# Performance work log

Measured on AMD Instinct MI355X. Metric: run time of the kernel, lower is better.

The kernel has to match this reference:

```python
import jax, jax.numpy as jnp
import numpy as np

B, SEQ, EMB, LAT = 8192, 1024, 768, 256
TAXA = ['phylum', 'order', 'family', 'genus', 'species']
NC = {'phylum': 40, 'order': 200, 'family': 800, 'genus': 3000, 'species': 12000}


def _table(P, C):
    # parent->child validity: child c belongs to parent (c % P); every parent non-empty
    return (jnp.arange(C)[None, :] % P) == jnp.arange(P)[:, None]


def setup_inputs() -> dict:
    key = jax.random.key(0)
    ks = jax.random.split(key, 16)
    d = {}
    d['sequences'] = jax.random.normal(ks[0], (B, SEQ), jnp.float32)
    d['W_dnabert'] = jax.random.normal(ks[1], (SEQ, EMB), jnp.float32) * 0.02
    d['W_enc'] = jax.random.normal(ks[2], (EMB, LAT), jnp.float32) * 0.02
    for i, t in enumerate(TAXA):
        d[f'W_cls_{t}'] = jax.random.normal(ks[3 + i], (LAT, NC[t]), jnp.float32) * 0.02
        d[f'W_dec_{t}'] = jax.random.normal(ks[8 + i], (LAT, EMB), jnp.float32) * 0.02
    d['W_global'] = jax.random.normal(ks[13], (LAT, EMB), jnp.float32) * 0.02
    d['T_order'] = _table(NC['phylum'], NC['order'])
    d['T_family'] = _table(NC['order'], NC['family'])
    d['T_genus'] = _table(NC['family'], NC['genus'])
    d['T_species'] = _table(NC['genus'], NC['species'])
    return d


def reference(sequences, W_dnabert, W_enc,
              W_cls_phylum, W_cls_order, W_cls_family, W_cls_genus, W_cls_species,
              W_dec_phylum, W_dec_order, W_dec_family, W_dec_genus, W_dec_species,
              W_global, T_order, T_family, T_genus, T_species):
    # frozen dnabert (torch.no_grad)
    emb = jax.lax.stop_gradient(sequences @ W_dnabert)          # [B, EMB]
    z = emb @ W_enc                                             # [B, LAT]

    Wc = {'phylum': W_cls_phylum, 'order': W_cls_order, 'family': W_cls_family,
          'genus': W_cls_genus, 'species': W_cls_species}
    Wd = {'phylum': W_dec_phylum, 'order': W_dec_order, 'family': W_dec_family,
          'genus': W_dec_genus, 'species': W_dec_species}
    Tt = {'order': T_order, 'family': T_family, 'genus': T_genus, 'species': T_species}

    logits_out, recon_out = {}, {}
    parent_preds = None
    for taxon in TAXA:
        logits = z @ Wc[taxon]                                  # [B, C_taxon]
        if parent_preds is not None and taxon in Tt:
            # vectorized hierarchical mask: gather valid-class row per sample
            mask = Tt[taxon][parent_preds]                      # [B, C_taxon] bool
            logits = jnp.where(mask, logits, -jnp.inf)
        logits_out[taxon] = logits
        recon_out[taxon] = z @ Wd[taxon]                        # [B, EMB]
        parent_preds = jnp.argmax(logits, axis=1)               # [B] int

    global_rec = z @ W_global                                   # [B, EMB]
    return (z,
            logits_out['phylum'], logits_out['order'], logits_out['family'],
            logits_out['genus'], logits_out['species'],
            recon_out['phylum'], recon_out['order'], recon_out['family'],
            recon_out['genus'], recon_out['species'],
            global_rec, emb)
```

## Files before the change

kernel.cpp:

```cpp
#include <hip/hip_runtime.h>
#include <hip/hip_bf16.h>

typedef __attribute__((ext_vector_type(8))) short short8;
typedef __attribute__((ext_vector_type(4))) float f32x4;
typedef unsigned short ushort_t;
typedef unsigned int u32;

static constexpr int Bn  = 8192;
static constexpr int SEQ = 1024;
static constexpr int EMB = 768;
static constexpr int LAT = 256;

static constexpr size_t OFF_Z   = 0;
static constexpr size_t OFF_LP  = 2097152;
static constexpr size_t OFF_LO  = 2424832;
static constexpr size_t OFF_LF  = 4063232;
static constexpr size_t OFF_LG  = 10616832;
static constexpr size_t OFF_LS  = 35192832;
static constexpr size_t OFF_RP  = 133496832;
static constexpr size_t OFF_EMB = 171245568;

static constexpr size_t SCR      = OFF_LO;
static constexpr size_t S_SEQ_H  = SCR + 0;
static constexpr size_t S_SEQ_L  = SCR + 4194304;
static constexpr size_t S_EMB_H  = SCR + 8388608;
static constexpr size_t S_EMB_L  = SCR + 11534336;
static constexpr size_t S_Z_H    = SCR + 14680064;
static constexpr size_t S_Z_L    = SCR + 15728640;
static constexpr size_t S_REC_H  = SCR + 16777216;
static constexpr size_t S_REC_L  = SCR + 17367040;
static constexpr size_t S_CLS_T  = SCR + 17956864;
static constexpr size_t S_T_O    = S_CLS_T + 0;
static constexpr size_t S_T_F    = S_CLS_T + 51200;
static constexpr size_t S_T_G    = S_CLS_T + 256000;
static constexpr size_t S_T_S    = S_CLS_T + 1024000;

static constexpr size_t SCR_END  = SCR + 22052864;
static constexpr size_t TE0 = 0,        TE1 = 9418752;
static constexpr size_t TZ0 = 9418752,  TZ1 = 18837504;
static constexpr size_t TR0 = 18837504, TR1 = 27254784;
static constexpr size_t FILLZ_N4 = 8388608 / 4;
static constexpr size_t FILLR_N4 = (14680064 - 8388608) / 4;
static constexpr size_t ZREC_N4  = (17956864 - 14680064) / 4;
static constexpr size_t CLST_N4  = (22052864 - 17956864) / 4;

static constexpr size_t WS_DNA_H = 0;
static constexpr size_t WS_DNA_L = 786432;
static constexpr size_t WS_ENC_H = 1572864;
static constexpr size_t WS_ENC_L = 1769472;
static constexpr size_t WS_COMPACT_FL = 983040;

#define MASKED_VAL (-1.0e30f)

__device__ __forceinline__ ushort_t bfbits(float f) {
    return __builtin_bit_cast(ushort_t, __float2bfloat16(f));
}
__device__ __forceinline__ float bf2f(ushort_t h) {
    return __builtin_bit_cast(float, ((unsigned)h) << 16);
}
__device__ __forceinline__ void split2(float f, ushort_t& h, ushort_t& l) {
    h = bfbits(f);
    l = bfbits(f - bf2f(h));
}

__device__ __forceinline__ size_t tile_pos(int rt, int nKT, int kt, int r, int g) {
    return ((size_t)rt * nKT + kt) * 8192 + (size_t)r * 64 + ((g ^ (r & 7)) << 3);
}

__device__ __forceinline__ void fill_span(f32x4* __restrict__ dst, size_t n4,
                                          int fb, int nFB)
{
    const f32x4 v = {MASKED_VAL, MASKED_VAL, MASKED_VAL, MASKED_VAL};
    for (size_t i = (size_t)fb * 256 + threadIdx.x; i < n4; i += (size_t)nFB * 256)
        __builtin_nontemporal_store(v, dst + i);
}

__global__ __launch_bounds__(256)
void fill_kernel(f32x4* __restrict__ dst, size_t n4)
{
    fill_span(dst, n4, blockIdx.x, gridDim.x);
}

__device__ __forceinline__ void prep_wtT_body(const float* __restrict__ src,
                                              ushort_t* __restrict__ dh,
                                              ushort_t* __restrict__ dl,
                                              int K, int N, int bx, int nb)
{
    const int gpr = K >> 3, nKT = K >> 6;
    const int nG = N * gpr;
    for (int gi = bx * 256 + threadIdx.x; gi < nG; gi += nb * 256) {
        const int n = gi / gpr, gk = gi - n * gpr;
        short8 hh, ll;
        #pragma unroll
        for (int j = 0; j < 8; ++j) {
            ushort_t hv, lv;
            split2(src[(size_t)(gk * 8 + j) * N + n], hv, lv);
            hh[j] = (short)hv; ll[j] = (short)lv;
        }
        const size_t base = tile_pos(n >> 7, nKT, gk >> 3, n & 127, gk & 7);
        *(short8*)(dh + base) = hh;
        *(short8*)(dl + base) = ll;
    }
}

struct Ptr6 { const float* p[6]; };

__device__ __forceinline__ void prep_rec_body(Ptr6 s, ushort_t* __restrict__ dh,
                                              ushort_t* __restrict__ dl, int bx, int nb)
{
    constexpr int gpr = 32, nKT = 4;
    const int nG = 4608 * gpr;
    for (int gi = bx * 256 + threadIdx.x; gi < nG; gi += nb * 256) {
        const int np = gi / gpr, gk = gi - np * gpr;
        const int m = np / 768, nn = np - m * 768;
        const float* sm = s.p[m];
        short8 hh, ll;
        #pragma unroll
        for (int j = 0; j < 8; ++j) {
            ushort_t hv, lv;
            split2(sm[(size_t)(gk * 8 + j) * 768 + nn], hv, lv);
            hh[j] = (short)hv; ll[j] = (short)lv;
        }
        const size_t base = tile_pos(np >> 7, nKT, gk >> 3, np & 127, gk & 7);
        *(short8*)(dh + base) = hh;
        *(short8*)(dl + base) = ll;
    }
}

__device__ __forceinline__ void transpose_body(float t[64][65], int bx,
    const float* __restrict__ Wo, const float* __restrict__ Wf,
    const float* __restrict__ Wg, const float* __restrict__ Ws,
    float* To, float* Tf, float* Tg, float* Ts)
{
    const float* src; float* dst; int C; int cb;
    if (bx < 16)       { src = Wo; dst = To; C = 200;   cb = bx; }
    else if (bx < 68)  { src = Wf; dst = Tf; C = 800;   cb = bx - 16; }
    else if (bx < 256) { src = Wg; dst = Tg; C = 3000;  cb = bx - 68; }
    else               { src = Ws; dst = Ts; C = 12000; cb = bx - 256; }
    const int ct = cb >> 2, kt = cb & 3;
    const int c0 = ct * 64;
    const int tid = threadIdx.x;
    const int cl = tid & 63, kr = tid >> 6;
    #pragma unroll
    for (int i = 0; i < 16; ++i) {
        const int k = i * 4 + kr;
        const int c = c0 + cl;
        t[k][cl] = (c < C) ? src[(size_t)(kt * 64 + k) * C + c] : 0.f;
    }
    __syncthreads();
    #pragma unroll
    for (int i = 0; i < 16; ++i) {
        const int cc = i * 4 + kr;
        const int c = c0 + cc;
        if (c < C) dst[(size_t)c * 256 + kt * 64 + cl] = t[cl][cc];
    }
}

__device__ __forceinline__ void split_body(const float* __restrict__ src,
                                           ushort_t* __restrict__ dh,
                                           ushort_t* __restrict__ dl,
                                           int M, int K, int bx, int nb)
{
    const int gpr = K >> 3, nKT = K >> 6;
    const int nG = M * gpr;
    for (int gi = bx * 256 + threadIdx.x; gi < nG; gi += nb * 256) {
        const int row = gi / gpr, gk = gi - row * gpr;
        const float* s = src + (size_t)row * K + gk * 8;
        const float4 a = *(const float4*)s;
        const float4 b = *(const float4*)(s + 4);
        const float f[8] = {a.x, a.y, a.z, a.w, b.x, b.y, b.z, b.w};
        short8 hh, ll;
        #pragma unroll
        for (int j = 0; j < 8; ++j) {
            ushort_t hv, lv;
            split2(f[j], hv, lv);
            hh[j] = (short)hv; ll[j] = (short)lv;
        }
        const size_t base = tile_pos(row >> 7, nKT, gk >> 3, row & 127, gk & 7);
        *(short8*)(dh + base) = hh;
        *(short8*)(dl + base) = ll;
    }
}

__global__ __launch_bounds__(256)
void prep_everything(const float* Wdna, ushort_t* dnaH, ushort_t* dnaL,
                     const float* Wenc, ushort_t* encH, ushort_t* encL,
                     Ptr6 s6, ushort_t* recH, ushort_t* recL,
                     const float* Wo, const float* Wf, const float* Wg, const float* Ws,
                     float* To, float* Tf, float* Tg, float* Ts,
                     const float* seq, ushort_t* seqH, ushort_t* seqL)
{
    __shared__ float t[64][65];
    const int bx = blockIdx.x;
    if (bx < 1056) {
        if (bx < 384)       prep_wtT_body(Wdna, dnaH, dnaL, 1024, 768, bx, 384);
        else if (bx < 480)  prep_wtT_body(Wenc, encH, encL, 768, 256, bx - 384, 96);
        else                prep_rec_body(s6, recH, recL, bx - 480, 576);
    } else if (bx < 2064) {
        transpose_body(t, bx - 1056, Wo, Wf, Wg, Ws, To, Tf, Tg, Ts);
    } else {
        split_body(seq, seqH, seqL, Bn, SEQ, bx - 2064, 4096);
    }
}

__device__ __forceinline__ void gload16(const ushort_t* g, ushort_t* l) {
    __builtin_amdgcn_global_load_lds(
        (const __attribute__((address_space(1))) u32*)g,
        (__attribute__((address_space(3))) u32*)l, 16, 0, 0);
}

__global__ __launch_bounds__(256)
void gemm_ts_fill(const ushort_t* __restrict__ Ahg, const ushort_t* __restrict__ Alg,
                  const ushort_t* __restrict__ Bhg, const ushort_t* __restrict__ Blg,
                  int K, float* __restrict__ Cbase, int chunkW, size_t chunkStride,
                  int nCT, int nGB,
                  f32x4* __restrict__ f1, size_t n1,
                  f32x4* __restrict__ f2, size_t n2)
{
    __shared__ ushort_t sAh[8192], sAl[8192], sBh[8192], sBl[8192];

    if ((int)blockIdx.x >= nGB) {
        const int fb = blockIdx.x - nGB, nFB = gridDim.x - nGB;
        fill_span(f1, n1, fb, nFB);
        if (n2) fill_span(f2, n2, fb, nFB);
        return;
    }

    const int tid = threadIdx.x, w = tid >> 6, lane = tid & 63;
    const int wm = w >> 1, wn = w & 1;
    const int fr = lane & 15, kg = lane >> 4;
    const int nKT = K >> 6;
    const int rt = blockIdx.x / nCT, ct = blockIdx.x % nCT;
    const int col0 = ct * 128;
    const int chunk = col0 / chunkW;
    const int lc0 = col0 - chunk * chunkW;
    float* __restrict__ C = Cbase + (size_t)chunk * chunkStride;

    const int sbase = w * 2048;
    const int lgo = lane * 8;

    f32x4 acc[4][4] = {};

    for (int kt = 0; kt < nKT; ++kt) {
        const size_t at = ((size_t)rt * nKT + kt) * 8192;
        const size_t bt = ((size_t)ct * nKT + kt) * 8192;
        #pragma unroll
        for (int i = 0; i < 4; ++i) {
            const int co = sbase + i * 512;
            gload16(Ahg + at + co + lgo, &sAh[co]);
            gload16(Alg + at + co + lgo, &sAl[co]);
            gload16(Bhg + bt + co + lgo, &sBh[co]);
            gload16(Blg + bt + co + lgo, &sBl[co]);
        }
        __syncthreads();

        #pragma unroll
        for (int ks = 0; ks < 2; ++ks) {
            const int g = ks * 4 + kg;
            short8 a_h[4], a_l[4], b_h[4], b_l[4];
            #pragma unroll
            for (int i = 0; i < 4; ++i) {
                const int ra = wm * 64 + i * 16 + fr;
                const int pa = ra * 64 + ((g ^ (ra & 7)) << 3);
                a_h[i] = *(const short8*)&sAh[pa];
                a_l[i] = *(const short8*)&sAl[pa];
                const int rb = wn * 64 + i * 16 + fr;
                const int pb = rb * 64 + ((g ^ (rb & 7)) << 3);
                b_h[i] = *(const short8*)&sBh[pb];
                b_l[i] = *(const short8*)&sBl[pb];
            }
            #pragma unroll
            for (int mi = 0; mi < 4; ++mi) {
                #pragma unroll
                for (int ni = 0; ni < 4; ++ni) {
                    acc[mi][ni] = __builtin_amdgcn_mfma_f32_16x16x32_bf16(a_h[mi], b_h[ni], acc[mi][ni], 0, 0, 0);
                    acc[mi][ni] = __builtin_amdgcn_mfma_f32_16x16x32_bf16(a_h[mi], b_l[ni], acc[mi][ni], 0, 0, 0);
                    acc[mi][ni] = __builtin_amdgcn_mfma_f32_16x16x32_bf16(a_l[mi], b_h[ni], acc[mi][ni], 0, 0, 0);
                }
            }
        }
        __syncthreads();
    }

    const int crow = kg * 4;
    #pragma unroll
    for (int mi = 0; mi < 4; ++mi) {
        const int gr = rt * 128 + wm * 64 + mi * 16 + crow;
        #pragma unroll
        for (int ni = 0; ni < 4; ++ni) {
            const int gc = lc0 + wn * 64 + ni * 16 + fr;
            #pragma unroll
            for (int j = 0; j < 4; ++j)
                C[(size_t)(gr + j) * chunkW + gc] = acc[mi][ni][j];
        }
    }
}

__global__ __launch_bounds__(256)
void split_tiled(const float* __restrict__ src, ushort_t* __restrict__ dh,
                 ushort_t* __restrict__ dl, int M, int K)
{
    split_body(src, dh, dl, M, K, blockIdx.x, gridDim.x);
}

template <int C, int P>
__device__ __forceinline__ int level_w(const float* __restrict__ WT,
                                       float4 zr, int p, int lane,
                                       float* __restrict__ rec )
{
    const int cnt = (C - p + P - 1) / P;
    float sv[5];
    #pragma unroll
    for (int j = 0; j < 5; ++j) {
        float s = 0.f;
        if (j < cnt) {
            const float4 wv = *(const float4*)(WT + (size_t)(p + j * P) * 256 + lane * 4);
            s = fmaf(wv.x, zr.x, fmaf(wv.y, zr.y, fmaf(wv.z, zr.z, wv.w * zr.w)));
        }
        sv[j] = s;
    }
    #pragma unroll
    for (int j = 0; j < 5; ++j) {
        if (j < cnt) {
            #pragma unroll
            for (int off = 32; off; off >>= 1) sv[j] += __shfl_xor(sv[j], off);
        }
    }
    float best = sv[0];
    int bj = 0;
    #pragma unroll
    for (int j = 1; j < 5; ++j)
        if (j < cnt && sv[j] > best) { best = sv[j]; bj = j; }

    if (lane == 0) {
        rec[0] = __int_as_float(p);
        rec[1] = sv[0];
        rec[2] = (1 < cnt) ? sv[1] : 0.f;
        rec[3] = (2 < cnt) ? sv[2] : 0.f;
        rec[4] = (3 < cnt) ? sv[3] : 0.f;
        rec[5] = (4 < cnt) ? sv[4] : 0.f;
    }
    return p + bj * P;
}

__device__ __forceinline__ void chain_body(float* zsh, int bid,
    const float* __restrict__ z, const float* __restrict__ Wp,
    const float* __restrict__ ToT, const float* __restrict__ TfT,
    const float* __restrict__ TgT, const float* __restrict__ TsT,
    float* __restrict__ out, float* __restrict__ compact)
{
    const int w    = threadIdx.x >> 6;
    const int lane = threadIdx.x & 63;
    const size_t b = (size_t)bid * 4 + w;

    const float4 zr4 = *(const float4*)(z + b * 256 + lane * 4);
    *(float4*)&zsh[w * 256 + lane * 4] = zr4;
    asm volatile("s_waitcnt lgkmcnt(0)" ::: "memory");
    const float* zrow = zsh + w * 256;

    float pv = MASKED_VAL;
    if (lane < 40) {
        float s0 = 0.f, s1 = 0.f, s2 = 0.f, s3 = 0.f;
        #pragma unroll 4
        for (int k = 0; k < 256; k += 4) {
            s0 = fmaf(zrow[k + 0], Wp[(k + 0) * 40 + lane], s0);
            s1 = fmaf(zrow[k + 1], Wp[(k + 1) * 40 + lane], s1);
            s2 = fmaf(zrow[k + 2], Wp[(k + 2) * 40 + lane], s2);
            s3 = fmaf(zrow[k + 3], Wp[(k + 3) * 40 + lane], s3);
        }
        pv = (s0 + s1) + (s2 + s3);
        out[OFF_LP + b * 40 + lane] = pv;
    }
    float v = pv;
    int idx = lane;
    #pragma unroll
    for (int off = 32; off; off >>= 1) {
        float ov = __shfl_xor(v, off);
        int   oi = __shfl_xor(idx, off);
        if (ov > v || (ov == v && oi < idx)) { v = ov; idx = oi; }
    }
    int p = idx;

    p = level_w<200, 40>    (ToT, zr4, p, lane, compact + (0 * Bn + b) * 6);
    p = level_w<800, 200>   (TfT, zr4, p, lane, compact + (1 * Bn + b) * 6);
    p = level_w<3000, 800>  (TgT, zr4, p, lane, compact + (2 * Bn + b) * 6);
    (void)level_w<12000, 3000>(TsT, zr4, p, lane, compact + (3 * Bn + b) * 6);
}

__global__ __launch_bounds__(256)
void chain_fill(const float* __restrict__ z, const float* __restrict__ Wp,
                const float* __restrict__ ToT, const float* __restrict__ TfT,
                const float* __restrict__ TgT, const float* __restrict__ TsT,
                float* __restrict__ out, float* __restrict__ compact,
                f32x4* __restrict__ f1, size_t n1)
{
    __shared__ float zsh[4 * 256];
    const int bx = blockIdx.x;
    if (bx >= Bn / 4) {
        fill_span(f1, n1, bx - Bn / 4, gridDim.x - Bn / 4);
        return;
    }
    chain_body(zsh, bx, z, Wp, ToT, TfT, TgT, TsT, out, compact);
}

__global__ __launch_bounds__(256)
void scatter_kernel(const float* __restrict__ compact, float* __restrict__ out)
{
    const int t = blockIdx.x * 256 + threadIdx.x;
    if (t >= 4 * Bn) return;
    const int lvl = t >> 13, b = t & (Bn - 1);
    const int Cs[4] = {200, 800, 3000, 12000};
    const int Ps[4] = {40, 200, 800, 3000};
    const size_t OFFL[4] = {OFF_LO, OFF_LF, OFF_LG, OFF_LS};
    const float* rec = compact + ((size_t)lvl * Bn + b) * 6;
    const int p = __float_as_int(rec[0]);
    const int C = Cs[lvl], P = Ps[lvl];
    const int cnt = (C - p + P - 1) / P;
    float* dst = out + OFFL[lvl] + (size_t)b * C;
    for (int j = 0; j < cnt; ++j)
        dst[p + j * P] = rec[1 + j];
}

extern "C" void kernel_launch(void* const* d_in, const int* in_sizes, int n_in,
                              void* d_out, int out_size, void* d_ws, size_t ws_size,
                              hipStream_t stream)
{
    const float* seq    = (const float*)d_in[0];
    const float* Wdna   = (const float*)d_in[1];
    const float* Wenc   = (const float*)d_in[2];
    const float* Wcls_p = (const float*)d_in[3];
    const float* Wdec_p = (const float*)d_in[4];
    const float* Wcls_o = (const float*)d_in[5];
    const float* Wdec_o = (const float*)d_in[6];
    const float* Wcls_f = (const float*)d_in[7];
    const float* Wdec_f = (const float*)d_in[8];
    const float* Wcls_g = (const float*)d_in[9];
    const float* Wdec_g = (const float*)d_in[10];
    const float* Wcls_s = (const float*)d_in[11];
    const float* Wdec_s = (const float*)d_in[12];
    const float* Wglob  = (const float*)d_in[13];
    (void)in_sizes; (void)n_in; (void)out_size; (void)ws_size;

    float* out = (float*)d_out;
    ushort_t* ws = (ushort_t*)d_ws;

    ushort_t* seqH = (ushort_t*)(out + S_SEQ_H);
    ushort_t* seqL = (ushort_t*)(out + S_SEQ_L);
    ushort_t* embH = (ushort_t*)(out + S_EMB_H);
    ushort_t* embL = (ushort_t*)(out + S_EMB_L);
    ushort_t* zH   = (ushort_t*)(out + S_Z_H);
    ushort_t* zL   = (ushort_t*)(out + S_Z_L);
    ushort_t* recH = (ushort_t*)(out + S_REC_H);
    ushort_t* recL = (ushort_t*)(out + S_REC_L);
    float* ToT = out + S_T_O;
    float* TfT = out + S_T_F;
    float* TgT = out + S_T_G;
    float* TsT = out + S_T_S;
    ushort_t* dnaH = ws + WS_DNA_H;
    ushort_t* dnaL = ws + WS_DNA_L;
    ushort_t* encH = ws + WS_ENC_H;
    ushort_t* encL = ws + WS_ENC_L;
    float* compact = (float*)ws + WS_COMPACT_FL;
    f32x4* tail = (f32x4*)(out + SCR_END);

    Ptr6 s6{{Wdec_p, Wdec_o, Wdec_f, Wdec_g, Wdec_s, Wglob}};
    prep_everything<<<6160, 256, 0, stream>>>(
        Wdna, dnaH, dnaL, Wenc, encH, encL, s6, recH, recL,
        Wcls_o, Wcls_f, Wcls_g, Wcls_s, ToT, TfT, TgT, TsT,
        seq, seqH, seqL);

    gemm_ts_fill<<<384 + 1664, 256, 0, stream>>>(
        seqH, seqL, dnaH, dnaL, SEQ, out + OFF_EMB, EMB, 0, 6, 384,
        tail + TE0, TE1 - TE0, nullptr, 0);
    split_tiled<<<3072, 256, 0, stream>>>(out + OFF_EMB, embH, embL, Bn, EMB);

    gemm_ts_fill<<<128 + 896, 256, 0, stream>>>(
        embH, embL, encH, encL, EMB, out + OFF_Z, LAT, 0, 2, 128,
        (f32x4*)(out + SCR), FILLZ_N4, tail + TZ0, TZ1 - TZ0);
    split_tiled<<<1024, 256, 0, stream>>>(out + OFF_Z, zH, zL, Bn, LAT);

    gemm_ts_fill<<<2304 + 768, 256, 0, stream>>>(
        zH, zL, recH, recL, LAT, out + OFF_RP, EMB, (size_t)Bn * EMB, 36, 2304,
        (f32x4*)(out + S_EMB_H), FILLR_N4, tail + TR0, TR1 - TR0);

    chain_fill<<<2048 + 512, 256, 0, stream>>>(out + OFF_Z, Wcls_p, ToT, TfT,
                                               TgT, TsT, out, compact,
                                               (f32x4*)(out + S_Z_H), ZREC_N4);

    fill_kernel<<<512, 256, 0, stream>>>((f32x4*)(out + S_CLS_T), CLST_N4);
    scatter_kernel<<<128, 256, 0, stream>>>(compact, out);
}
```

Baseline: 304.8 us.

## Swizzle GEMM block order, nontemporal recon stores, merge fill into scatter

```diff
diff --git a/kernel.cpp b/kernel.cpp
--- a/kernel.cpp
+++ b/kernel.cpp
@@ -213,7 +213,7 @@
 void gemm_ts_fill(const ushort_t* __restrict__ Ahg, const ushort_t* __restrict__ Alg,
                   const ushort_t* __restrict__ Bhg, const ushort_t* __restrict__ Blg,
                   int K, float* __restrict__ Cbase, int chunkW, size_t chunkStride,
-                  int nCT, int nGB,
+                  int nCT, int nGB, int ntC,
                   f32x4* __restrict__ f1, size_t n1,
                   f32x4* __restrict__ f2, size_t n2)
 {
@@ -226,11 +226,13 @@
         return;
     }
 
+    const int bx = (blockIdx.x & 7) * (nGB >> 3) + (blockIdx.x >> 3);
+
     const int tid = threadIdx.x, w = tid >> 6, lane = tid & 63;
     const int wm = w >> 1, wn = w & 1;
     const int fr = lane & 15, kg = lane >> 4;
     const int nKT = K >> 6;
-    const int rt = blockIdx.x / nCT, ct = blockIdx.x % nCT;
+    const int rt = bx / nCT, ct = bx % nCT;
     const int col0 = ct * 128;
     const int chunk = col0 / chunkW;
     const int lc0 = col0 - chunk * chunkW;
@@ -289,9 +291,16 @@
         #pragma unroll
         for (int ni = 0; ni < 4; ++ni) {
             const int gc = lc0 + wn * 64 + ni * 16 + fr;
-            #pragma unroll
-            for (int j = 0; j < 4; ++j)
-                C[(size_t)(gr + j) * chunkW + gc] = acc[mi][ni][j];
+            if (ntC) {
+                #pragma unroll
+                for (int j = 0; j < 4; ++j)
+                    __builtin_nontemporal_store(acc[mi][ni][j],
+                        &C[(size_t)(gr + j) * chunkW + gc]);
+            } else {
+                #pragma unroll
+                for (int j = 0; j < 4; ++j)
+                    C[(size_t)(gr + j) * chunkW + gc] = acc[mi][ni][j];
+            }
         }
     }
 }
@@ -404,9 +413,15 @@
 }
 
 __global__ __launch_bounds__(256)
-void scatter_kernel(const float* __restrict__ compact, float* __restrict__ out)
-{
-    const int t = blockIdx.x * 256 + threadIdx.x;
+void scatter_fill(const float* __restrict__ compact, float* __restrict__ out,
+                  f32x4* __restrict__ f1, size_t n1)
+{
+    const int bx = blockIdx.x;
+    if (bx >= 128) {
+        fill_span(f1, n1, bx - 128, gridDim.x - 128);
+        return;
+    }
+    const int t = bx * 256 + threadIdx.x;
     if (t >= 4 * Bn) return;
     const int lvl = t >> 13, b = t & (Bn - 1);
     const int Cs[4] = {200, 800, 3000, 12000};
@@ -470,23 +485,23 @@
         seq, seqH, seqL);
 
     gemm_ts_fill<<<384 + 1664, 256, 0, stream>>>(
-        seqH, seqL, dnaH, dnaL, SEQ, out + OFF_EMB, EMB, 0, 6, 384,
+        seqH, seqL, dnaH, dnaL, SEQ, out + OFF_EMB, EMB, 0, 6, 384, 0,
         tail + TE0, TE1 - TE0, nullptr, 0);
     split_tiled<<<3072, 256, 0, stream>>>(out + OFF_EMB, embH, embL, Bn, EMB);
 
     gemm_ts_fill<<<128 + 896, 256, 0, stream>>>(
-        embH, embL, encH, encL, EMB, out + OFF_Z, LAT, 0, 2, 128,
+        embH, embL, encH, encL, EMB, out + OFF_Z, LAT, 0, 2, 128, 0,
         (f32x4*)(out + SCR), FILLZ_N4, tail + TZ0, TZ1 - TZ0);
     split_tiled<<<1024, 256, 0, stream>>>(out + OFF_Z, zH, zL, Bn, LAT);
 
     gemm_ts_fill<<<2304 + 768, 256, 0, stream>>>(
-        zH, zL, recH, recL, LAT, out + OFF_RP, EMB, (size_t)Bn * EMB, 36, 2304,
+        zH, zL, recH, recL, LAT, out + OFF_RP, EMB, (size_t)Bn * EMB, 36, 2304, 1,
         (f32x4*)(out + S_EMB_H), FILLR_N4, tail + TR0, TR1 - TR0);
 
     chain_fill<<<2048 + 512, 256, 0, stream>>>(out + OFF_Z, Wcls_p, ToT, TfT,
                                                TgT, TsT, out, compact,
                                                (f32x4*)(out + S_Z_H), ZREC_N4);
 
-    fill_kernel<<<512, 256, 0, stream>>>((f32x4*)(out + S_CLS_T), CLST_N4);
-    scatter_kernel<<<128, 256, 0, stream>>>(compact, out);
-}
+    scatter_fill<<<128 + 512, 256, 0, stream>>>(compact, out,
+                                                (f32x4*)(out + S_CLS_T), CLST_N4);
+}
```

New measurement: 295.6 us. 1.03x faster.
